# Kernel tuning notes

Hardware: AMD Instinct MI355X
Metric: run time of the kernel (lower is better)

The kernel has to match this reference:

```python
import jax, jax.numpy as jnp
import numpy as np

N_NODES = 100000
N_EDGES = 1600000
NUM_GRAPHS = 64
EPS = 1e-5


def setup_inputs() -> dict:
    key = jax.random.key(0)
    ks = jax.random.split(key, 8)
    x = jax.random.normal(ks[0], (N_NODES, 64), dtype=jnp.float32)
    edge_index = jax.random.randint(ks[1], (2, N_EDGES), 0, N_NODES, dtype=jnp.int64)
    batch = jnp.sort(jax.random.randint(ks[2], (N_NODES,), 0, NUM_GRAPHS, dtype=jnp.int64))
    conv_W = jax.random.normal(ks[3], (2, 64, 64), dtype=jnp.float32) * (1.0 / np.sqrt(64))
    conv_b = jnp.zeros((2, 64), jnp.float32)
    bn_gamma = jnp.ones((2, 64), jnp.float32)
    bn_beta = jnp.zeros((2, 64), jnp.float32)
    bn_mean = jnp.zeros((2, 64), jnp.float32)
    bn_var = jnp.ones((2, 64), jnp.float32)
    head_W = jax.random.normal(ks[4], (3, 64, 16), dtype=jnp.float32) * (1.0 / np.sqrt(64))
    head_b = jnp.zeros((3, 16), jnp.float32)
    return {"x": x, "edge_index": edge_index, "batch": batch,
            "conv_W": conv_W, "conv_b": conv_b,
            "bn_gamma": bn_gamma, "bn_beta": bn_beta,
            "bn_mean": bn_mean, "bn_var": bn_var,
            "head_W": head_W, "head_b": head_b}


def _gcn_forward(x, edge_index, batch, conv_W, conv_b, bn_gamma, bn_beta, bn_mean, bn_var, head_W, head_b):
    src, dst = edge_index[0], edge_index[1]
    # symmetric GCN normalization with added self-loops (PyG GCNConv default)
    deg = jax.ops.segment_sum(jnp.ones((N_EDGES,), x.dtype), dst, num_segments=N_NODES) + 1.0
    dinv = jax.lax.rsqrt(deg)                      # [N]
    enorm = (dinv[src] * dinv[dst])[:, None]       # [E,1]
    selfnorm = (dinv * dinv)[:, None]              # [N,1]

    def gcn_conv(h, W, b):
        h = h @ W                                  # [N,d]
        agg = jax.ops.segment_sum(h[src] * enorm, dst, num_segments=N_NODES)
        return agg + h * selfnorm + b

    def bn_relu(h, l):
        inv = jax.lax.rsqrt(bn_var[l] + EPS)
        return jax.nn.relu((h - bn_mean[l]) * inv * bn_gamma[l] + bn_beta[l])

    hidden_rep = [x]
    h = x
    for l in range(2):  # num_layers - 1
        h = gcn_conv(h, conv_W[l], conv_b[l])
        h = bn_relu(h, l)
        hidden_rep.append(h)

    score = jnp.zeros((NUM_GRAPHS, 16), x.dtype)
    for l, hr in enumerate(hidden_rep):
        pooled = jax.ops.segment_sum(hr, batch, num_segments=NUM_GRAPHS)  # global_add_pool
        score = score + pooled @ head_W[l] + head_b[l]                    # dropout off (eval)
    return score


def reference(x, edge_index, batch, conv_W, conv_b, bn_gamma, bn_beta, bn_mean, bn_var, head_W, head_b):
    return _gcn_forward(x, edge_index, batch, conv_W, conv_b, bn_gamma, bn_beta, bn_mean, bn_var, head_W, head_b)
```

## Files before the change

### kernel.cpp

```cpp
#include <hip/hip_runtime.h>
#include <hip/hip_fp16.h>

#define N_NODES    100000
#define N_EDGES    1600000
#define NUM_GRAPHS 64
#define F          64
#define EPS        1e-5f
#define DEG_CAP    64
#define BIN_NODES  512
#define NBINS      ((N_NODES + BIN_NODES - 1) / BIN_NODES)
#define BIN_CAP    16000
#define KB_BLOCKS  128
#define KB_EDGES   (N_EDGES / KB_BLOCKS)

typedef __attribute__((ext_vector_type(8))) _Float16 f16x8;
typedef __attribute__((ext_vector_type(4))) float    f32x4;

__global__ void k_init(float* pooled, int* binCnt) {
    int i = blockIdx.x * blockDim.x + threadIdx.x;
    if (i < 3 * NUM_GRAPHS * F) pooled[i] = 0.f;
    if (i < NBINS) binCnt[i] = 0;
}

__global__ void k_bin(const int* __restrict__ src, const int* __restrict__ dst,
                      int* __restrict__ binCnt, int2* __restrict__ bins) {
    __shared__ int bcnt[NBINS];
    __shared__ int bbase[NBINS];
    __shared__ int brun[NBINS];
    int t = threadIdx.x;
    for (int i = t; i < NBINS; i += 256) bcnt[i] = 0;
    __syncthreads();
    size_t e0 = (size_t)blockIdx.x * KB_EDGES;
    const int4* d4 = (const int4*)(dst + e0);
    const int4* s4 = (const int4*)(src + e0);
    const int NV = KB_EDGES / 4;
    for (int i = t; i < NV; i += 256) {
        int4 dv = d4[i];
        atomicAdd(&bcnt[dv.x / BIN_NODES], 1);
        atomicAdd(&bcnt[dv.y / BIN_NODES], 1);
        atomicAdd(&bcnt[dv.z / BIN_NODES], 1);
        atomicAdd(&bcnt[dv.w / BIN_NODES], 1);
    }
    __syncthreads();
    for (int i = t; i < NBINS; i += 256) {
        bbase[i] = atomicAdd(&binCnt[i], bcnt[i]);
        brun[i] = 0;
    }
    __syncthreads();
    for (int i = t; i < NV; i += 256) {
        int4 dv = d4[i];
        int4 sv = s4[i];
#define DO_E(dd, ss)                                                         \
        {                                                                    \
            int bn = (dd) / BIN_NODES;                                       \
            int r = atomicAdd(&brun[bn], 1);                                 \
            int off = bbase[bn] + r;                                         \
            if (off < BIN_CAP) bins[(size_t)bn * BIN_CAP + off] = make_int2((ss), (dd)); \
        }
        DO_E(dv.x, sv.x) DO_E(dv.y, sv.y) DO_E(dv.z, sv.z) DO_E(dv.w, sv.w)
#undef DO_E
    }
}

__global__ void __launch_bounds__(256, 1) k_fill3(const int* __restrict__ binCnt,
                        const int2* __restrict__ bins,
                        int* __restrict__ cnt, int* __restrict__ bucket) {
    __shared__ int lbucket[BIN_NODES * DEG_CAP];
    __shared__ int lcnt[BIN_NODES];
    int bn = blockIdx.x;
    int base = bn * BIN_NODES;
    int nnodes = N_NODES - base; if (nnodes > BIN_NODES) nnodes = BIN_NODES;
    int t = threadIdx.x;
    for (int i = t; i < BIN_NODES; i += 256) lcnt[i] = 0;
    __syncthreads();
    int n = binCnt[bn]; if (n > BIN_CAP) n = BIN_CAP;
    const int2* bin = bins + (size_t)bn * BIN_CAP;
    for (int i = t; i < n; i += 256) {
        int2 e = bin[i];
        int slot = atomicAdd(&lcnt[e.y - base], 1);
        if (slot < DEG_CAP) lbucket[(e.y - base) * DEG_CAP + slot] = e.x;
    }
    __syncthreads();
    int4* gb = (int4*)(bucket + (size_t)base * DEG_CAP);
    const int4* lb = (const int4*)lbucket;
    int nv = nnodes * (DEG_CAP / 4);
    for (int i = t; i < nv; i += 256) gb[i] = lb[i];
    for (int i = t; i < nnodes; i += 256) cnt[base + i] = lcnt[i];
}

#define N_TILES (N_NODES / 16)
#define GT_BLOCKS ((N_TILES + 3) / 4)
__global__ void k_gemm_mfma(const float* __restrict__ h, const float* __restrict__ W,
                            const int* __restrict__ cnt, __half* __restrict__ out) {
    __shared__ _Float16 Wh[64 * 64];
    int t = threadIdx.x;
    for (int i = t; i < 64 * 64; i += 256) Wh[i] = (_Float16)W[i];
    __syncthreads();
    int lane = t & 63, wv = t >> 6;
    int tile = blockIdx.x * 4 + wv;
    if (tile >= N_TILES) return;
    int row0 = tile * 16;
    int r   = lane & 15;
    int g16 = lane >> 4;
    int k0  = g16 * 8;

    f16x8 Bf[4][2];
#pragma unroll
    for (int ct = 0; ct < 4; ++ct)
#pragma unroll
        for (int ck = 0; ck < 2; ++ck)
#pragma unroll
            for (int i = 0; i < 8; ++i)
                Bf[ct][ck][i] = Wh[(32 * ck + k0 + i) * 64 + ct * 16 + r];

    f16x8 Af[2];
#pragma unroll
    for (int ck = 0; ck < 2; ++ck) {
        const float4* x4 = (const float4*)(h + (size_t)(row0 + r) * F + 32 * ck + k0);
        float4 p = x4[0], q = x4[1];
        Af[ck][0] = (_Float16)p.x; Af[ck][1] = (_Float16)p.y;
        Af[ck][2] = (_Float16)p.z; Af[ck][3] = (_Float16)p.w;
        Af[ck][4] = (_Float16)q.x; Af[ck][5] = (_Float16)q.y;
        Af[ck][6] = (_Float16)q.z; Af[ck][7] = (_Float16)q.w;
    }

    f32x4 acc[4];
#pragma unroll
    for (int ct = 0; ct < 4; ++ct) {
        f32x4 z = {0.f, 0.f, 0.f, 0.f};
        acc[ct] = __builtin_amdgcn_mfma_f32_16x16x32_f16(Af[0], Bf[ct][0], z, 0, 0, 0);
        acc[ct] = __builtin_amdgcn_mfma_f32_16x16x32_f16(Af[1], Bf[ct][1], acc[ct], 0, 0, 0);
    }

#pragma unroll
    for (int j = 0; j < 4; ++j) {
        int rr = row0 + 4 * g16 + j;
        float di = rsqrtf((float)cnt[rr] + 1.0f);
#pragma unroll
        for (int ct = 0; ct < 4; ++ct)
            out[(size_t)rr * F + ct * 16 + r] = __float2half(acc[ct][j] * di);
    }
}

__device__ __forceinline__ float2 cvt2(unsigned int u) {
    __half2 h = *reinterpret_cast<__half2*>(&u);
    return __half22float2(h);
}

#define ACC8(u, wt)                                                          \
    {                                                                        \
        float2 p0 = cvt2((u).x), p1 = cvt2((u).y),                           \
               p2 = cvt2((u).z), p3 = cvt2((u).w);                           \
        a0 = fmaf(p0.x, wt, a0); a1 = fmaf(p0.y, wt, a1);                    \
        a2 = fmaf(p1.x, wt, a2); a3 = fmaf(p1.y, wt, a3);                    \
        a4 = fmaf(p2.x, wt, a4); a5 = fmaf(p2.y, wt, a5);                    \
        a6 = fmaf(p3.x, wt, a6); a7 = fmaf(p3.y, wt, a7);                    \
    }

template<bool WRITE_OUT, bool POOL_X>
__global__ void k_agg_pool(const __half* __restrict__ hs, const int* __restrict__ cnt,
                           const int* __restrict__ bucket,
                           const int* __restrict__ batch,
                           const float* __restrict__ x,
                           const float* __restrict__ b, const float* __restrict__ gamma,
                           const float* __restrict__ beta, const float* __restrict__ mean,
                           const float* __restrict__ var,
                           float* __restrict__ out,
                           float* __restrict__ pooledX, float* __restrict__ pooledV) {
    __shared__ float prowV[16][64];
    __shared__ float prowX[16][64];
    __shared__ int pg[16];
    int w    = threadIdx.x >> 6;
    int lane = threadIdx.x & 63;
    int sub  = lane & 15;
    int nsel = lane >> 4;
    int esel = sub >> 3;
    int q    = sub & 7;
    int base = lane & 48;
    int nodeIdx = w * 4 + nsel;
    int d = blockIdx.x * 16 + nodeIdx;
    const uint4* hs4 = (const uint4*)hs;

    int cdeg = cnt[d];
    int kk = cdeg > (DEG_CAP - 1) ? (DEG_CAP - 1) : cdeg;
    int nentF = kk + 1;
    int ev0 = (sub == 0) ? d : bucket[(size_t)d * DEG_CAP + sub - 1];
    int ev1 = bucket[(size_t)d * DEG_CAP + 15 + sub];
    float4 xv = make_float4(0.f, 0.f, 0.f, 0.f);
    if (POOL_X) xv = ((const float4*)x)[(size_t)d * 16 + sub];
    int g = batch[d];

    float a0 = 0.f, a1 = 0.f, a2 = 0.f, a3 = 0.f,
          a4 = 0.f, a5 = 0.f, a6 = 0.f, a7 = 0.f;

#define SELA(i) int s##i; float w##i;                                        \
    { int t = 2 * (i) + esel; int c = __shfl(ev0, base + t);                 \
      s##i = (t < nentF) ? c : d; w##i = (t < nentF) ? 1.f : 0.f; }
#define SELB(i) int s##i; float w##i;                                        \
    { int t = 2 * (i) + esel; int c = __shfl(ev1, base + (t - 16));          \
      s##i = (t < nentF) ? c : d; w##i = (t < nentF) ? 1.f : 0.f; }
#define LD(i) uint4 u##i = hs4[(size_t)s##i * 8 + q];

    SELA(0) SELA(1) SELA(2) SELA(3) SELA(4) SELA(5) SELA(6) SELA(7)
    SELB(8) SELB(9) SELB(10) SELB(11) SELB(12) SELB(13) SELB(14) SELB(15)
    LD(0) LD(1) LD(2) LD(3) LD(4) LD(5) LD(6) LD(7)
    LD(8) LD(9) LD(10) LD(11) LD(12) LD(13) LD(14) LD(15)
    ACC8(u0,  w0)  ACC8(u1,  w1)  ACC8(u2,  w2)  ACC8(u3,  w3)
    ACC8(u4,  w4)  ACC8(u5,  w5)  ACC8(u6,  w6)  ACC8(u7,  w7)
    ACC8(u8,  w8)  ACC8(u9,  w9)  ACC8(u10, w10) ACC8(u11, w11)
    ACC8(u12, w12) ACC8(u13, w13) ACC8(u14, w14) ACC8(u15, w15)
#undef SELA
#undef SELB
#undef LD

    if (__any(nentF > 32)) {
        int evA = bucket[(size_t)d * DEG_CAP + 31 + sub];
        int evB = bucket[(size_t)d * DEG_CAP + 47 + sub];
#pragma unroll
        for (int i = 0; i < 16; ++i) {
            int t = 32 + 2 * i + esel;
            int cA = __shfl(evA, base + ((t - 32) & 15));
            int cB = __shfl(evB, base + ((t - 48) & 15));
            int c = (t < 48) ? cA : cB;
            int s = (t < nentF) ? c : d;
            uint4 uu = hs4[(size_t)s * 8 + q];
            float wt = (t < nentF) ? 1.f : 0.f;
            ACC8(uu, wt);
        }
    }

    a0 += __shfl_xor(a0, 8); a1 += __shfl_xor(a1, 8);
    a2 += __shfl_xor(a2, 8); a3 += __shfl_xor(a3, 8);
    a4 += __shfl_xor(a4, 8); a5 += __shfl_xor(a5, 8);
    a6 += __shfl_xor(a6, 8); a7 += __shfl_xor(a7, 8);

    if (sub < 8) {
        float di = rsqrtf((float)cdeg + 1.0f);
        const float4* b4  = (const float4*)b;
        const float4* m4  = (const float4*)mean;
        const float4* v4  = (const float4*)var;
        const float4* g4  = (const float4*)gamma;
        const float4* e4  = (const float4*)beta;
        float4 bb0 = b4[2 * q], bb1 = b4[2 * q + 1];
        float4 mm0 = m4[2 * q], mm1 = m4[2 * q + 1];
        float4 vv0 = v4[2 * q], vv1 = v4[2 * q + 1];
        float4 gg0 = g4[2 * q], gg1 = g4[2 * q + 1];
        float4 ee0 = e4[2 * q], ee1 = e4[2 * q + 1];
        float4 V0, V1;
        V0.x = fmaxf((di * a0 + bb0.x - mm0.x) * rsqrtf(vv0.x + EPS) * gg0.x + ee0.x, 0.f);
        V0.y = fmaxf((di * a1 + bb0.y - mm0.y) * rsqrtf(vv0.y + EPS) * gg0.y + ee0.y, 0.f);
        V0.z = fmaxf((di * a2 + bb0.z - mm0.z) * rsqrtf(vv0.z + EPS) * gg0.z + ee0.z, 0.f);
        V0.w = fmaxf((di * a3 + bb0.w - mm0.w) * rsqrtf(vv0.w + EPS) * gg0.w + ee0.w, 0.f);
        V1.x = fmaxf((di * a4 + bb1.x - mm1.x) * rsqrtf(vv1.x + EPS) * gg1.x + ee1.x, 0.f);
        V1.y = fmaxf((di * a5 + bb1.y - mm1.y) * rsqrtf(vv1.y + EPS) * gg1.y + ee1.y, 0.f);
        V1.z = fmaxf((di * a6 + bb1.z - mm1.z) * rsqrtf(vv1.z + EPS) * gg1.z + ee1.z, 0.f);
        V1.w = fmaxf((di * a7 + bb1.w - mm1.w) * rsqrtf(vv1.w + EPS) * gg1.w + ee1.w, 0.f);
        if (WRITE_OUT) {
            float4* o4 = (float4*)out;
            o4[(size_t)d * 16 + 2 * q]     = V0;
            o4[(size_t)d * 16 + 2 * q + 1] = V1;
        }
        float4* pv = (float4*)&prowV[nodeIdx][0];
        pv[2 * q]     = V0;
        pv[2 * q + 1] = V1;
    }
    if (POOL_X) ((float4*)&prowX[nodeIdx][0])[sub] = xv;
    if (sub == 0) pg[nodeIdx] = g;
    __syncthreads();

    int f2 = threadIdx.x & 63;
    for (int r = threadIdx.x >> 6; r < 16; r += 4) {
        int gg = pg[r];
        bool first = true;
        for (int r2 = 0; r2 < r; ++r2) if (pg[r2] == gg) first = false;
        if (first) {
            float a = 0.f, bx = 0.f;
            for (int r2 = r; r2 < 16; ++r2)
                if (pg[r2] == gg) { a += prowV[r2][f2]; if (POOL_X) bx += prowX[r2][f2]; }
            atomicAdd(&pooledV[gg * F + f2], a);
            if (POOL_X) atomicAdd(&pooledX[gg * F + f2], bx);
        }
    }
}

__global__ void k_head(const float* __restrict__ pooled, const float* __restrict__ headW,
                       const float* __restrict__ headb, float* __restrict__ out) {
    int idx = blockIdx.x * blockDim.x + threadIdx.x;
    if (idx >= NUM_GRAPHS * 16) return;
    int g = idx >> 4, o = idx & 15;
    float acc = 0.f;
#pragma unroll
    for (int l = 0; l < 3; ++l) {
        const float* pl = pooled + (size_t)l * NUM_GRAPHS * F + (size_t)g * F;
        const float* wl = headW + (size_t)l * F * 16;
        float s = 0.f;
        for (int k = 0; k < F; ++k) s += pl[k] * wl[k * 16 + o];
        acc += s + headb[l * 16 + o];
    }
    out[idx] = acc;
}

extern "C" void kernel_launch(void* const* d_in, const int* in_sizes, int n_in,
                              void* d_out, int out_size, void* d_ws, size_t ws_size,
                              hipStream_t stream) {
    const float* x     = (const float*)d_in[0];
    const int*   ei    = (const int*)d_in[1];
    const int*   src   = ei;
    const int*   dst   = ei + N_EDGES;
    const int*   batch = (const int*)d_in[2];
    const float* convW = (const float*)d_in[3];
    const float* convb = (const float*)d_in[4];
    const float* gamma = (const float*)d_in[5];
    const float* beta  = (const float*)d_in[6];
    const float* mean  = (const float*)d_in[7];
    const float* var   = (const float*)d_in[8];
    const float* headW = (const float*)d_in[9];
    const float* headb = (const float*)d_in[10];
    float* out = (float*)d_out;

    char* p = (char*)d_ws;
    int*    cnt    = (int*)p;       p += sizeof(int) * N_NODES;
    int*    bucket = (int*)p;       p += sizeof(int) * (size_t)N_NODES * DEG_CAP;
    __half* hs     = (__half*)p;    p += sizeof(__half) * (size_t)N_NODES * F;
    float*  hA     = (float*)p;     p += sizeof(float) * (size_t)N_NODES * F;
    float*  pooled = (float*)p;     p += sizeof(float) * 3 * NUM_GRAPHS * F;
    int*    binCnt = (int*)p;       p += sizeof(int) * NBINS;
    int2*   bins   = (int2*)hA;

    const int B = 256;
    int gN   = (N_NODES + B - 1) / B;
    int gAgg = N_NODES / 16;

    k_init <<<gN, B, 0, stream>>>(pooled, binCnt);
    k_bin  <<<KB_BLOCKS, B, 0, stream>>>(src, dst, binCnt, bins);
    k_fill3<<<NBINS, B, 0, stream>>>(binCnt, bins, cnt, bucket);

    k_gemm_mfma<<<GT_BLOCKS, B, 0, stream>>>(x, convW, cnt, hs);
    k_agg_pool<true, true><<<gAgg, B, 0, stream>>>(hs, cnt, bucket, batch, x, convb,
                                                   gamma, beta, mean, var,
                                                   hA, pooled, pooled + NUM_GRAPHS * F);

    k_gemm_mfma<<<GT_BLOCKS, B, 0, stream>>>(hA, convW + F * F, cnt, hs);
    k_agg_pool<false, false><<<gAgg, B, 0, stream>>>(hs, cnt, bucket, batch, nullptr,
                                                     convb + F, gamma + F, beta + F,
                                                     mean + F, var + F,
                                                     nullptr, nullptr,
                                                     pooled + 2 * NUM_GRAPHS * F);

    k_head<<<(NUM_GRAPHS * 16 + B - 1) / B, B, 0, stream>>>(pooled, headW, headb, out);
}
```

Before: 165.2 us.

## Fuse second-layer GEMM into first aggregation kernel epilogue using MFMA

```diff
diff --git a/kernel.cpp b/kernel.cpp
--- a/kernel.cpp
+++ b/kernel.cpp
@@ -157,7 +157,7 @@
         a6 = fmaf(p3.x, wt, a6); a7 = fmaf(p3.y, wt, a7);                    \
     }
 
-template<bool WRITE_OUT, bool POOL_X>
+template<bool POOL_X, bool DO_GEMM>
 __global__ void k_agg_pool(const __half* __restrict__ hs, const int* __restrict__ cnt,
                            const int* __restrict__ bucket,
                            const int* __restrict__ batch,
@@ -165,13 +165,15 @@
                            const float* __restrict__ b, const float* __restrict__ gamma,
                            const float* __restrict__ beta, const float* __restrict__ mean,
                            const float* __restrict__ var,
-                           float* __restrict__ out,
+                           const float* __restrict__ W1, __half* __restrict__ hs_next,
                            float* __restrict__ pooledX, float* __restrict__ pooledV) {
     __shared__ float prowV[16][64];
     __shared__ float prowX[16][64];
+    __shared__ _Float16 Wh[64 * 64];
     __shared__ int pg[16];
-    int w    = threadIdx.x >> 6;
-    int lane = threadIdx.x & 63;
+    int tid  = threadIdx.x;
+    int w    = tid >> 6;
+    int lane = tid & 63;
     int sub  = lane & 15;
     int nsel = lane >> 4;
     int esel = sub >> 3;
@@ -180,6 +182,9 @@
     int nodeIdx = w * 4 + nsel;
     int d = blockIdx.x * 16 + nodeIdx;
     const uint4* hs4 = (const uint4*)hs;
+
+    if (DO_GEMM)
+        for (int i = tid; i < 64 * 64; i += 256) Wh[i] = (_Float16)W1[i];
 
     int cdeg = cnt[d];
     int kk = cdeg > (DEG_CAP - 1) ? (DEG_CAP - 1) : cdeg;
@@ -255,11 +260,6 @@
         V1.y = fmaxf((di * a5 + bb1.y - mm1.y) * rsqrtf(vv1.y + EPS) * gg1.y + ee1.y, 0.f);
         V1.z = fmaxf((di * a6 + bb1.z - mm1.z) * rsqrtf(vv1.z + EPS) * gg1.z + ee1.z, 0.f);
         V1.w = fmaxf((di * a7 + bb1.w - mm1.w) * rsqrtf(vv1.w + EPS) * gg1.w + ee1.w, 0.f);
-        if (WRITE_OUT) {
-            float4* o4 = (float4*)out;
-            o4[(size_t)d * 16 + 2 * q]     = V0;
-            o4[(size_t)d * 16 + 2 * q + 1] = V1;
-        }
         float4* pv = (float4*)&prowV[nodeIdx][0];
         pv[2 * q]     = V0;
         pv[2 * q + 1] = V1;
@@ -268,8 +268,8 @@
     if (sub == 0) pg[nodeIdx] = g;
     __syncthreads();
 
-    int f2 = threadIdx.x & 63;
-    for (int r = threadIdx.x >> 6; r < 16; r += 4) {
+    int f2 = tid & 63;
+    for (int r = tid >> 6; r < 16; r += 4) {
         int gg = pg[r];
         bool first = true;
         for (int r2 = 0; r2 < r; ++r2) if (pg[r2] == gg) first = false;
@@ -279,6 +279,29 @@
                 if (pg[r2] == gg) { a += prowV[r2][f2]; if (POOL_X) bx += prowX[r2][f2]; }
             atomicAdd(&pooledV[gg * F + f2], a);
             if (POOL_X) atomicAdd(&pooledX[gg * F + f2], bx);
+        }
+    }
+
+    if (DO_GEMM) {
+        int r   = lane & 15;
+        int g16 = lane >> 4;
+        int k0  = g16 * 8;
+        f16x8 Af[2], Bf[2];
+#pragma unroll
+        for (int ck = 0; ck < 2; ++ck)
+#pragma unroll
+            for (int i = 0; i < 8; ++i) {
+                Af[ck][i] = (_Float16)prowV[r][32 * ck + k0 + i];
+                Bf[ck][i] = Wh[(32 * ck + k0 + i) * 64 + w * 16 + r];
+            }
+        f32x4 z = {0.f, 0.f, 0.f, 0.f};
+        f32x4 acc = __builtin_amdgcn_mfma_f32_16x16x32_f16(Af[0], Bf[0], z, 0, 0, 0);
+        acc = __builtin_amdgcn_mfma_f32_16x16x32_f16(Af[1], Bf[1], acc, 0, 0, 0);
+#pragma unroll
+        for (int j = 0; j < 4; ++j) {
+            int rr = blockIdx.x * 16 + 4 * g16 + j;
+            float di = rsqrtf((float)cnt[rr] + 1.0f);
+            hs_next[(size_t)rr * F + w * 16 + r] = __float2half(acc[j] * di);
         }
     }
 }
@@ -322,30 +345,31 @@
     int*    cnt    = (int*)p;       p += sizeof(int) * N_NODES;
     int*    bucket = (int*)p;       p += sizeof(int) * (size_t)N_NODES * DEG_CAP;
     __half* hs     = (__half*)p;    p += sizeof(__half) * (size_t)N_NODES * F;
-    float*  hA     = (float*)p;     p += sizeof(float) * (size_t)N_NODES * F;
+    char*   hAreg  = p;             p += sizeof(float) * (size_t)N_NODES * F;
     float*  pooled = (float*)p;     p += sizeof(float) * 3 * NUM_GRAPHS * F;
     int*    binCnt = (int*)p;       p += sizeof(int) * NBINS;
-    int2*   bins   = (int2*)hA;
+    int2*   bins   = (int2*)hAreg;
+    __half* hs1    = (__half*)hAreg;
 
     const int B = 256;
-    int gN   = (N_NODES + B - 1) / B;
-    int gAgg = N_NODES / 16;
-
-    k_init <<<gN, B, 0, stream>>>(pooled, binCnt);
+    int gInit = (3 * NUM_GRAPHS * F + B - 1) / B;
+    int gAgg  = N_NODES / 16;
+
+    k_init <<<gInit, B, 0, stream>>>(pooled, binCnt);
     k_bin  <<<KB_BLOCKS, B, 0, stream>>>(src, dst, binCnt, bins);
     k_fill3<<<NBINS, B, 0, stream>>>(binCnt, bins, cnt, bucket);
 
     k_gemm_mfma<<<GT_BLOCKS, B, 0, stream>>>(x, convW, cnt, hs);
     k_agg_pool<true, true><<<gAgg, B, 0, stream>>>(hs, cnt, bucket, batch, x, convb,
                                                    gamma, beta, mean, var,
-                                                   hA, pooled, pooled + NUM_GRAPHS * F);
-
-    k_gemm_mfma<<<GT_BLOCKS, B, 0, stream>>>(hA, convW + F * F, cnt, hs);
-    k_agg_pool<false, false><<<gAgg, B, 0, stream>>>(hs, cnt, bucket, batch, nullptr,
+                                                   convW + F * F, hs1,
+                                                   pooled, pooled + NUM_GRAPHS * F);
+
+    k_agg_pool<false, false><<<gAgg, B, 0, stream>>>(hs1, cnt, bucket, batch, nullptr,
                                                      convb + F, gamma + F, beta + F,
                                                      mean + F, var + F,
                                                      nullptr, nullptr,
-                                                     pooled + 2 * NUM_GRAPHS * F);
+                                                     nullptr, pooled + 2 * NUM_GRAPHS * F);
 
     k_head<<<(NUM_GRAPHS * 16 + B - 1) / B, B, 0, stream>>>(pooled, headW, headb, out);
 }
```

Result: faster. 156.7 us (-5.1%).
